# Kernel optimization log

Hardware: AMD Instinct MI355X
Metric: run time of the kernel (lower is better)

Reference implementation:

```python
import jax, jax.numpy as jnp
import numpy as np
from jax import lax

# Model constants (from init_kwargs)
N_B, N_T, N_IN, N_REC, N_OUT = 64, 1000, 80, 512, 20
DT, TAU_M, TAU_O = 1.0, 20.0, 20.0
ALPHA = float(np.exp(-DT / TAU_M))   # membrane leak
KAPPA = float(np.exp(-DT / TAU_O))   # output leak
THR = 1.0
B_O = 0.0
GAIN = (0.5, 0.1, 0.5)


def setup_inputs() -> dict:
    key = jax.random.key(0)
    k = jax.random.split(key, 5)
    x = jax.random.normal(k[0], (N_B, N_T, N_IN), jnp.float32)
    # kaiming_normal_ (fan_in mode, std = sqrt(2/fan_in)) scaled by gain
    w_in = jax.random.normal(k[1], (N_REC, N_IN), jnp.float32) * (np.sqrt(2.0 / N_IN) * GAIN[0])
    w_rec = jax.random.normal(k[2], (N_REC, N_REC), jnp.float32) * (np.sqrt(2.0 / N_REC) * GAIN[1])
    w_out = jax.random.normal(k[3], (N_OUT, N_REC), jnp.float32) * (np.sqrt(2.0 / N_REC) * GAIN[2])
    # per-step torch.randn noise, materialized deterministically
    noise = jax.random.normal(k[4], (N_T, N_B, N_REC), jnp.float32)
    # full-length sequences: pack/pad roundtrip becomes identity
    seq_lengths = jnp.full((N_B,), N_T, dtype=jnp.int32)
    return {"x": x, "w_in": w_in, "w_rec": w_rec, "w_out": w_out,
            "noise": noise, "seq_lengths": seq_lengths}


def reference(x, w_in, w_rec, w_out, noise, seq_lengths):
    """LIF spiking RNN forward (inference path, do_training=False).

    x:     (B, T, n_in)
    noise: (T, B, n_rec)  -- the per-step torch.randn injected into v
    Returns (softmax_vo (B,T,n_out), vo (T,B,n_out)) as in the torch module.
    """
    n_b, n_t, _ = x.shape
    n_rec = w_rec.shape[0]
    n_out = w_out.shape[0]
    dtype = x.dtype

    # zero the recurrent self-connections (w_rec *= 1 - eye)
    w_rec_m = w_rec * (1.0 - jnp.eye(n_rec, dtype=w_rec.dtype))

    # padded inputs are zero beyond seq_lengths; here all lengths == n_t so
    # the pack/pad roundtrip is identity. mask anyway for faithfulness.
    t_idx = jnp.arange(n_t)[None, :, None]                     # (1,T,1)
    x_padded = jnp.where(t_idx < seq_lengths[:, None, None], x, 0.0)

    def step(carry, inp):
        v, z, vo = carry
        x_t, noise_t1 = inp
        # v[t+1] = alpha*v[t] + z[t]@w_rec.T + x[t]@w_in.T - z[t]*thr + noise
        v_new = (ALPHA * v
                 + z @ w_rec_m.T
                 + x_t @ w_in.T
                 - z * THR
                 + noise_t1)
        z_new = (v_new > THR).astype(dtype)          # hard threshold spike
        vo_new = KAPPA * vo + z_new @ w_out.T + B_O  # leaky readout
        return (v_new, z_new, vo_new), vo_new

    init = (jnp.zeros((n_b, n_rec), dtype),
            jnp.zeros((n_b, n_rec), dtype),
            jnp.zeros((n_b, n_out), dtype))
    # loop t = 0 .. n_t-2 consumes x[:, t] and noise[t+1]
    xs = (jnp.swapaxes(x_padded, 0, 1)[:-1], noise[1:])
    _, vo_seq = lax.scan(step, init, xs)             # (T-1, B, n_out)

    vo = jnp.concatenate([jnp.zeros((1, n_b, n_out), dtype), vo_seq], axis=0)  # (T,B,O)
    softmax_vo = jax.nn.softmax(jnp.transpose(vo, (1, 0, 2)), axis=2)          # (B,T,O)
    return softmax_vo, vo
```

## Files before the change

kernel.cpp:

```cpp
#include <hip/hip_runtime.h>

#define N_B   64
#define N_T   1000
#define N_IN  80
#define N_REC 512
#define N_OUT 20
#define THR 1.0f

constexpr float ALPHA = 0.9512294245007140f;
constexpr float KAPPA = 0.9512294245007140f;

__global__ void k_transpose(const float* __restrict__ w_rec, float* __restrict__ wT) {
    int i = blockIdx.x * blockDim.x + threadIdx.x;
    if (i >= 513 * N_REC) return;
    int j = i >> 9;
    int r = i & 511;
    float v = 0.0f;
    if (j < N_REC && r != j) v = w_rec[r * N_REC + j];
    wT[i] = v;
}

__global__ __launch_bounds__(512, 2) void k_inj(
    const float* __restrict__ x, const float* __restrict__ w_in,
    const float* __restrict__ noise, const int* __restrict__ seq,
    float* __restrict__ inj, int t0, int t1)
{
    const int r = threadIdx.x;
    float wreg[N_IN];
#pragma unroll
    for (int i = 0; i < N_IN; ++i) wreg[i] = w_in[r * N_IN + i];

    const int P = (t1 - t0) * N_B;
    const int stride = gridDim.x;

    auto nz = [&](int p) -> float {
        int pt = p >> 6, b = p & 63, t = t0 + pt;
        return __builtin_nontemporal_load(noise + ((size_t)t * N_B + b) * N_REC + r);
    };

    int p = blockIdx.x;
    float nxt = (p < P) ? nz(p) : 0.0f;
    for (; p < P; p += stride) {
        float acc = nxt;
        if (p + stride < P) nxt = nz(p + stride);
        int pt = p >> 6;
        int b  = p & 63;
        int t  = t0 + pt;
        if (t - 1 < seq[b]) {
            const float* xr = x + ((size_t)b * N_T + (t - 1)) * N_IN;
#pragma unroll
            for (int i = 0; i < N_IN; ++i) acc = fmaf(wreg[i], xr[i], acc);
        }
        inj[(size_t)p * N_REC + r] = acc;
    }
}

__global__ __launch_bounds__(512, 1) void k_scan(
    const float* __restrict__ wT, const float* __restrict__ inj,
    const float* __restrict__ w_out, float* __restrict__ out_vo,
    int t0, int t1,
    float* __restrict__ st_v, unsigned long long* __restrict__ st_zm,
    float* __restrict__ st_vo)
{
    const int b    = blockIdx.x;
    const int tid  = threadIdx.x;
    const int w    = tid >> 6;
    const int lane = tid & 63;
    const int g    = tid >> 7;
    const int c    = tid & 127;
    const unsigned long long lt = (1ull << lane) - 1ull;
    const int DUMMY = N_REC << 11;

    __shared__ int lists[N_REC];
    __shared__ unsigned long long zm[8];
    __shared__ int pc[8];
    __shared__ float4 tmp_part[4][128];
    __shared__ float tmp2[16][21];
    __shared__ alignas(16) float zfp[16 * 36];

    float wvo[32];
    {
        int o = tid >> 4, s = tid & 15;
        if (tid < 320) {
#pragma unroll
            for (int i = 0; i < 32; ++i)
                wvo[i] = w_out[(size_t)o * N_REC + s * 32 + i];
        } else {
#pragma unroll
            for (int i = 0; i < 32; ++i) wvo[i] = 0.0f;
        }
    }

    float v;
    int z;
    float vo = 0.0f;
    int npad = 0;

    if (t0 == 1) {
        v = 0.0f; z = 0;
    } else {
        v = st_v[(size_t)b * N_REC + tid];
        unsigned long long m = st_zm[b * 8 + w];
        z = (int)((m >> lane) & 1ull);
        if (tid < 8) zm[tid] = st_zm[b * 8 + tid];
        if (tid < N_OUT) vo = st_vo[b * N_OUT + tid];
        __syncthreads();
        unsigned long long bm0 = zm[w];
        if (lane == 0) pc[w] = __popcll(bm0);
        __syncthreads();
        int basep = 0, ntot = 0;
#pragma unroll
        for (int ww = 0; ww < 8; ++ww) {
            int s_ = pc[ww];
            if (ww < w) basep += s_;
            ntot += s_;
        }
        if (z) lists[basep + __popcll(bm0 & lt)] = tid << 11;
        npad = (ntot + 31) & ~31;
        { int i = ntot + tid; if (i < npad) lists[i] = DUMMY; }
        __syncthreads();
    }

    float injn = __builtin_nontemporal_load(inj + ((size_t)0 * N_B + b) * N_REC + tid);

    for (int t = t0; t < t1; ++t) {
        float injv = injn;

        float4 acc; acc.x = 0.0f; acc.y = 0.0f; acc.z = 0.0f; acc.w = 0.0f;
        {
            const int q = npad >> 2;
            if (q > 0) {
                int jv  = lists[g * q + lane];
                int jv2 = (q > 64) ? lists[g * q + 64 + (lane & 63)] : 0;
                const char* wb = (const char*)wT + (c << 4);
                const int nb = q >> 3;
                float4 vA[8];
#pragma unroll
                for (int u = 0; u < 8; ++u) {
                    int off = __builtin_amdgcn_readlane(jv, u);
                    vA[u] = *(const float4*)(wb + off);
                }
                for (int k = 1; k < nb; ++k) {
                    float4 vB[8];
#pragma unroll
                    for (int u = 0; u < 8; ++u) {
                        int ug = (k << 3) + u;
                        int off = (ug < 64)
                            ? __builtin_amdgcn_readlane(jv,  ug)
                            : __builtin_amdgcn_readlane(jv2, ug - 64);
                        vB[u] = *(const float4*)(wb + off);
                    }
#pragma unroll
                    for (int u = 0; u < 8; ++u) {
                        acc.x += vA[u].x; acc.y += vA[u].y;
                        acc.z += vA[u].z; acc.w += vA[u].w;
                        vA[u] = vB[u];
                    }
                }
#pragma unroll
                for (int u = 0; u < 8; ++u) {
                    acc.x += vA[u].x; acc.y += vA[u].y;
                    acc.z += vA[u].z; acc.w += vA[u].w;
                }
            }
        }
        if (t > t0 && tid < 320) {
            int o = tid >> 4, s = tid & 15;
            const float4* zp = (const float4*)(zfp + s * 36);
            float sa = 0.0f;
#pragma unroll
            for (int i = 0; i < 8; ++i) {
                float4 zv = zp[i];
                sa = fmaf(wvo[4 * i + 0], zv.x, sa);
                sa = fmaf(wvo[4 * i + 1], zv.y, sa);
                sa = fmaf(wvo[4 * i + 2], zv.z, sa);
                sa = fmaf(wvo[4 * i + 3], zv.w, sa);
            }
            tmp2[s][o] = sa;
        }
        tmp_part[g][c] = acc;

        if (t + 1 < t1)
            injn = __builtin_nontemporal_load(
                inj + ((size_t)(t + 1 - t0) * N_B + b) * N_REC + tid);

        __syncthreads();

        {
            const float* tp = (const float*)tmp_part;
            float accn = tp[tid] + tp[512 + tid] + tp[1024 + tid] + tp[1536 + tid];
            v = ALPHA * v + accn + injv - (z ? THR : 0.0f);
            z = v > THR;
            zfp[(tid >> 5) * 36 + (tid & 31)] = z ? 1.0f : 0.0f;
        }
        unsigned long long bm = __ballot(z);
        if (lane == 0) { zm[w] = bm; pc[w] = __popcll(bm); }
        if (t > t0 && tid < N_OUT) {
            float s = 0.0f;
#pragma unroll
            for (int ss = 0; ss < 16; ++ss) s += tmp2[ss][tid];
            vo = KAPPA * vo + s;
            out_vo[((size_t)(t - 1) * N_B + b) * N_OUT + tid] = vo;
        }
        __syncthreads();

        {
            int basep = 0, ntot = 0;
#pragma unroll
            for (int ww = 0; ww < 8; ++ww) {
                int s_ = pc[ww];
                if (ww < w) basep += s_;
                ntot += s_;
            }
            if (z) lists[basep + __popcll(bm & lt)] = tid << 11;
            int npn = (ntot + 31) & ~31;
            { int i = ntot + tid; if (i < npn) lists[i] = DUMMY; }
            npad = npn;
        }
        __syncthreads();
    }

    if (tid < 320) {
        int o = tid >> 4, s = tid & 15;
        const float4* zp = (const float4*)(zfp + s * 36);
        float sa = 0.0f;
#pragma unroll
        for (int i = 0; i < 8; ++i) {
            float4 zv = zp[i];
            sa = fmaf(wvo[4 * i + 0], zv.x, sa);
            sa = fmaf(wvo[4 * i + 1], zv.y, sa);
            sa = fmaf(wvo[4 * i + 2], zv.z, sa);
            sa = fmaf(wvo[4 * i + 3], zv.w, sa);
        }
        tmp2[s][o] = sa;
    }
    __syncthreads();
    if (tid < N_OUT) {
        float s = 0.0f;
#pragma unroll
        for (int ss = 0; ss < 16; ++ss) s += tmp2[ss][tid];
        vo = KAPPA * vo + s;
        out_vo[((size_t)(t1 - 1) * N_B + b) * N_OUT + tid] = vo;
        st_vo[b * N_OUT + tid] = vo;
    }

    st_v[(size_t)b * N_REC + tid] = v;
    if (lane == 0) st_zm[b * 8 + w] = zm[w];
}

__global__ void k_softmax(const float* __restrict__ vo_seq,
                          float* __restrict__ out_sm,
                          float* __restrict__ out_vo0)
{
    int idx = blockIdx.x * blockDim.x + threadIdx.x;
    if (idx >= N_B * N_T) return;
    int b = idx / N_T;
    int t = idx - b * N_T;
    float vals[N_OUT];
    if (t == 0) {
#pragma unroll
        for (int o = 0; o < N_OUT; ++o) {
            vals[o] = 0.0f;
            out_vo0[(size_t)b * N_OUT + o] = 0.0f;
        }
    } else {
#pragma unroll
        for (int o = 0; o < N_OUT; ++o)
            vals[o] = vo_seq[((size_t)t * N_B + b) * N_OUT + o];
    }
    float mx = vals[0];
#pragma unroll
    for (int o = 1; o < N_OUT; ++o) mx = fmaxf(mx, vals[o]);
    float s = 0.0f;
#pragma unroll
    for (int o = 0; o < N_OUT; ++o) { vals[o] = expf(vals[o] - mx); s += vals[o]; }
    float inv = 1.0f / s;
#pragma unroll
    for (int o = 0; o < N_OUT; ++o)
        out_sm[((size_t)b * N_T + t) * N_OUT + o] = vals[o] * inv;
}

extern "C" void kernel_launch(void* const* d_in, const int* in_sizes, int n_in,
                              void* d_out, int out_size, void* d_ws, size_t ws_size,
                              hipStream_t stream)
{
    (void)in_sizes; (void)n_in; (void)out_size;
    const float* x     = (const float*)d_in[0];
    const float* w_in  = (const float*)d_in[1];
    const float* w_rec = (const float*)d_in[2];
    const float* w_out = (const float*)d_in[3];
    const float* noise = (const float*)d_in[4];
    const int*   seq   = (const int*)d_in[5];

    float* out    = (float*)d_out;
    float* out_sm = out;
    float* out_vo = out + (size_t)N_B * N_T * N_OUT;

    char* ws = (char*)d_ws;
    float* wT = (float*)ws;
    size_t off = (size_t)513 * N_REC * sizeof(float);
    float* st_v = (float*)(ws + off);                off += (size_t)N_B * N_REC * sizeof(float);
    unsigned long long* st_zm = (unsigned long long*)(ws + off); off += (size_t)N_B * 8 * sizeof(unsigned long long);
    float* st_vo = (float*)(ws + off);               off += (size_t)N_B * N_OUT * sizeof(float);
    off = (off + 255) & ~(size_t)255;
    float* inj = (float*)(ws + off);

    size_t avail = (ws_size > off) ? (ws_size - off) : 0;
    size_t step_bytes = (size_t)N_B * N_REC * sizeof(float);
    long max_steps = (long)(avail / step_bytes);
    int tchunk = (int)((max_steps > (N_T - 1)) ? (N_T - 1) : max_steps);
    if (tchunk < 1) tchunk = 1;

    k_transpose<<<dim3((513 * N_REC + 255) / 256), dim3(256), 0, stream>>>(w_rec, wT);

    for (int t0 = 1; t0 < N_T; t0 += tchunk) {
        int t1 = t0 + tchunk; if (t1 > N_T) t1 = N_T;
        k_inj<<<dim3(512), dim3(512), 0, stream>>>(x, w_in, noise, seq, inj, t0, t1);
        k_scan<<<dim3(N_B), dim3(512), 0, stream>>>(wT, inj, w_out, out_vo,
                                                    t0, t1, st_v, st_zm, st_vo);
    }

    k_softmax<<<dim3((N_B * N_T + 255) / 256), dim3(256), 0, stream>>>(out_vo, out_sm, out_vo);
}
```

Baseline: 2.625 ms.

## Split each batch row's recurrent scan across two blocks with spike-mask exchange

```diff
diff --git a/kernel.cpp b/kernel.cpp
--- a/kernel.cpp
+++ b/kernel.cpp
@@ -10,8 +10,10 @@
 constexpr float ALPHA = 0.9512294245007140f;
 constexpr float KAPPA = 0.9512294245007140f;
 
-__global__ void k_transpose(const float* __restrict__ w_rec, float* __restrict__ wT) {
+__global__ void k_transpose(const float* __restrict__ w_rec, float* __restrict__ wT,
+                            unsigned long long* __restrict__ ex) {
     int i = blockIdx.x * blockDim.x + threadIdx.x;
+    if (i < 64 * 2 * 2 * 8) ex[i] = 0ull;
     if (i >= 513 * N_REC) return;
     int j = i >> 9;
     int r = i & 511;
@@ -60,113 +62,108 @@
     const float* __restrict__ w_out, float* __restrict__ out_vo,
     int t0, int t1,
     float* __restrict__ st_v, unsigned long long* __restrict__ st_zm,
-    float* __restrict__ st_vo)
+    float* __restrict__ st_vo, unsigned long long* __restrict__ ex)
 {
-    const int b    = blockIdx.x;
+    const int bid  = blockIdx.x;
+    const int b    = bid & 63;
+    const int sh   = bid >> 6;
+    const int cbase = sh << 8;
     const int tid  = threadIdx.x;
     const int w    = tid >> 6;
     const int lane = tid & 63;
-    const int g    = tid >> 7;
-    const int c    = tid & 127;
     const unsigned long long lt = (1ull << lane) - 1ull;
     const int DUMMY = N_REC << 11;
 
     __shared__ int lists[N_REC];
     __shared__ unsigned long long zm[8];
-    __shared__ int pc[8];
-    __shared__ float4 tmp_part[4][128];
+    __shared__ float4 tmp_part[8][64];
     __shared__ float tmp2[16][21];
     __shared__ alignas(16) float zfp[16 * 36];
 
     float wvo[32];
     {
-        int o = tid >> 4, s = tid & 15;
+        int o = tid >> 4, s16 = tid & 15;
         if (tid < 320) {
 #pragma unroll
             for (int i = 0; i < 32; ++i)
-                wvo[i] = w_out[(size_t)o * N_REC + s * 32 + i];
+                wvo[i] = w_out[(size_t)o * N_REC + s16 * 32 + i];
         } else {
 #pragma unroll
             for (int i = 0; i < 32; ++i) wvo[i] = 0.0f;
         }
     }
 
-    float v;
-    int z;
+    float v = 0.0f;
+    int zloc = 0;
     float vo = 0.0f;
     int npad = 0;
 
-    if (t0 == 1) {
-        v = 0.0f; z = 0;
-    } else {
-        v = st_v[(size_t)b * N_REC + tid];
-        unsigned long long m = st_zm[b * 8 + w];
-        z = (int)((m >> lane) & 1ull);
+    if (t0 > 1) {
+        if (tid < 256) v = st_v[(size_t)b * N_REC + cbase + tid];
         if (tid < 8) zm[tid] = st_zm[b * 8 + tid];
-        if (tid < N_OUT) vo = st_vo[b * N_OUT + tid];
-        __syncthreads();
-        unsigned long long bm0 = zm[w];
-        if (lane == 0) pc[w] = __popcll(bm0);
-        __syncthreads();
+        if (tid >= 256 && tid < 256 + N_OUT) vo = st_vo[b * N_OUT + (tid - 256)];
+        __syncthreads();
+        if (tid < 256)
+            zloc = (int)((zm[(cbase + tid) >> 6] >> (tid & 63)) & 1ull);
         int basep = 0, ntot = 0;
 #pragma unroll
         for (int ww = 0; ww < 8; ++ww) {
-            int s_ = pc[ww];
-            if (ww < w) basep += s_;
-            ntot += s_;
-        }
-        if (z) lists[basep + __popcll(bm0 & lt)] = tid << 11;
+            int c_ = __popcll(zm[ww]);
+            if (ww < w) basep += c_;
+            ntot += c_;
+        }
+        unsigned long long bmw = zm[w];
+        if ((bmw >> lane) & 1ull) lists[basep + __popcll(bmw & lt)] = tid << 11;
         npad = (ntot + 31) & ~31;
         { int i = ntot + tid; if (i < npad) lists[i] = DUMMY; }
         __syncthreads();
     }
 
-    float injn = __builtin_nontemporal_load(inj + ((size_t)0 * N_B + b) * N_REC + tid);
+    float injn = 0.0f;
+    if (tid < 256)
+        injn = __builtin_nontemporal_load(
+            inj + ((size_t)0 * N_B + b) * N_REC + cbase + tid);
 
     for (int t = t0; t < t1; ++t) {
         float injv = injn;
 
         float4 acc; acc.x = 0.0f; acc.y = 0.0f; acc.z = 0.0f; acc.w = 0.0f;
         {
-            const int q = npad >> 2;
+            const int q = npad >> 3;
             if (q > 0) {
-                int jv  = lists[g * q + lane];
-                int jv2 = (q > 64) ? lists[g * q + 64 + (lane & 63)] : 0;
-                const char* wb = (const char*)wT + (c << 4);
-                const int nb = q >> 3;
-                float4 vA[8];
-#pragma unroll
-                for (int u = 0; u < 8; ++u) {
+                int jv = lists[w * q + lane];
+                const char* wb = (const char*)wT + (sh << 10) + (lane << 4);
+                const int nb = q >> 2;
+                float4 vA[4];
+#pragma unroll
+                for (int u = 0; u < 4; ++u) {
                     int off = __builtin_amdgcn_readlane(jv, u);
                     vA[u] = *(const float4*)(wb + off);
                 }
-                for (int k = 1; k < nb; ++k) {
-                    float4 vB[8];
-#pragma unroll
-                    for (int u = 0; u < 8; ++u) {
-                        int ug = (k << 3) + u;
-                        int off = (ug < 64)
-                            ? __builtin_amdgcn_readlane(jv,  ug)
-                            : __builtin_amdgcn_readlane(jv2, ug - 64);
+                for (int kb = 1; kb < nb; ++kb) {
+                    float4 vB[4];
+#pragma unroll
+                    for (int u = 0; u < 4; ++u) {
+                        int off = __builtin_amdgcn_readlane(jv, (kb << 2) + u);
                         vB[u] = *(const float4*)(wb + off);
                     }
 #pragma unroll
-                    for (int u = 0; u < 8; ++u) {
+                    for (int u = 0; u < 4; ++u) {
                         acc.x += vA[u].x; acc.y += vA[u].y;
                         acc.z += vA[u].z; acc.w += vA[u].w;
                         vA[u] = vB[u];
                     }
                 }
 #pragma unroll
-                for (int u = 0; u < 8; ++u) {
+                for (int u = 0; u < 4; ++u) {
                     acc.x += vA[u].x; acc.y += vA[u].y;
                     acc.z += vA[u].z; acc.w += vA[u].w;
                 }
             }
         }
         if (t > t0 && tid < 320) {
-            int o = tid >> 4, s = tid & 15;
-            const float4* zp = (const float4*)(zfp + s * 36);
+            int o = tid >> 4, s16 = tid & 15;
+            const float4* zp = (const float4*)(zfp + s16 * 36);
             float sa = 0.0f;
 #pragma unroll
             for (int i = 0; i < 8; ++i) {
@@ -176,31 +173,52 @@
                 sa = fmaf(wvo[4 * i + 2], zv.z, sa);
                 sa = fmaf(wvo[4 * i + 3], zv.w, sa);
             }
-            tmp2[s][o] = sa;
-        }
-        tmp_part[g][c] = acc;
-
-        if (t + 1 < t1)
+            tmp2[s16][o] = sa;
+        }
+        tmp_part[w][lane] = acc;
+
+        if (tid < 256 && t + 1 < t1)
             injn = __builtin_nontemporal_load(
-                inj + ((size_t)(t + 1 - t0) * N_B + b) * N_REC + tid);
-
-        __syncthreads();
-
-        {
+                inj + ((size_t)(t + 1 - t0) * N_B + b) * N_REC + cbase + tid);
+
+        __syncthreads();
+
+        if (tid < 256) {
             const float* tp = (const float*)tmp_part;
-            float accn = tp[tid] + tp[512 + tid] + tp[1024 + tid] + tp[1536 + tid];
-            v = ALPHA * v + accn + injv - (z ? THR : 0.0f);
-            z = v > THR;
-            zfp[(tid >> 5) * 36 + (tid & 31)] = z ? 1.0f : 0.0f;
-        }
-        unsigned long long bm = __ballot(z);
-        if (lane == 0) { zm[w] = bm; pc[w] = __popcll(bm); }
-        if (t > t0 && tid < N_OUT) {
-            float s = 0.0f;
-#pragma unroll
-            for (int ss = 0; ss < 16; ++ss) s += tmp2[ss][tid];
-            vo = KAPPA * vo + s;
-            out_vo[((size_t)(t - 1) * N_B + b) * N_OUT + tid] = vo;
+            float accn = injv;
+#pragma unroll
+            for (int gg = 0; gg < 8; ++gg) accn += tp[gg * 256 + tid];
+            v = ALPHA * v + accn - (zloc ? THR : 0.0f);
+            zloc = v > THR;
+        }
+        unsigned long long bm = __ballot(zloc);
+        if (w < 4 && lane == 0) zm[sh * 4 + w] = bm;
+        __syncthreads();
+
+        if (tid == 0) {
+            const int par = t & 1;
+            unsigned long long* myslot = ex + (size_t)(((((b << 1) | sh) << 1) | par) * 8);
+            unsigned long long* pslot  = ex + (size_t)(((((b << 1) | (1 - sh)) << 1) | par) * 8);
+            unsigned long long w0 = zm[sh * 4 + 0], w1 = zm[sh * 4 + 1];
+            unsigned long long w2 = zm[sh * 4 + 2], w3 = zm[sh * 4 + 3];
+            __hip_atomic_store(myslot + 0, w0, __ATOMIC_RELAXED, __HIP_MEMORY_SCOPE_AGENT);
+            __hip_atomic_store(myslot + 1, w1, __ATOMIC_RELAXED, __HIP_MEMORY_SCOPE_AGENT);
+            __hip_atomic_store(myslot + 2, w2, __ATOMIC_RELAXED, __HIP_MEMORY_SCOPE_AGENT);
+            __hip_atomic_store(myslot + 3, w3, __ATOMIC_RELAXED, __HIP_MEMORY_SCOPE_AGENT);
+            __hip_atomic_store(myslot + 4, (unsigned long long)t,
+                               __ATOMIC_RELEASE, __HIP_MEMORY_SCOPE_AGENT);
+            while (__hip_atomic_load(pslot + 4, __ATOMIC_ACQUIRE,
+                                     __HIP_MEMORY_SCOPE_AGENT) < (unsigned long long)t) {}
+            zm[(1 - sh) * 4 + 0] = __hip_atomic_load(pslot + 0, __ATOMIC_RELAXED, __HIP_MEMORY_SCOPE_AGENT);
+            zm[(1 - sh) * 4 + 1] = __hip_atomic_load(pslot + 1, __ATOMIC_RELAXED, __HIP_MEMORY_SCOPE_AGENT);
+            zm[(1 - sh) * 4 + 2] = __hip_atomic_load(pslot + 2, __ATOMIC_RELAXED, __HIP_MEMORY_SCOPE_AGENT);
+            zm[(1 - sh) * 4 + 3] = __hip_atomic_load(pslot + 3, __ATOMIC_RELAXED, __HIP_MEMORY_SCOPE_AGENT);
+        } else if (tid >= 256 && tid < 256 + N_OUT && t > t0) {
+            float sum = 0.0f;
+#pragma unroll
+            for (int ss = 0; ss < 16; ++ss) sum += tmp2[ss][tid - 256];
+            vo = KAPPA * vo + sum;
+            out_vo[((size_t)(t - 1) * N_B + b) * N_OUT + (tid - 256)] = vo;
         }
         __syncthreads();
 
@@ -208,21 +226,24 @@
             int basep = 0, ntot = 0;
 #pragma unroll
             for (int ww = 0; ww < 8; ++ww) {
-                int s_ = pc[ww];
-                if (ww < w) basep += s_;
-                ntot += s_;
+                int c_ = __popcll(zm[ww]);
+                if (ww < w) basep += c_;
+                ntot += c_;
             }
-            if (z) lists[basep + __popcll(bm & lt)] = tid << 11;
+            unsigned long long bmw = zm[w];
+            if ((bmw >> lane) & 1ull) lists[basep + __popcll(bmw & lt)] = tid << 11;
             int npn = (ntot + 31) & ~31;
             { int i = ntot + tid; if (i < npn) lists[i] = DUMMY; }
             npad = npn;
+            zfp[(tid >> 5) * 36 + (tid & 31)] =
+                ((zm[tid >> 6] >> (tid & 63)) & 1ull) ? 1.0f : 0.0f;
         }
         __syncthreads();
     }
 
     if (tid < 320) {
-        int o = tid >> 4, s = tid & 15;
-        const float4* zp = (const float4*)(zfp + s * 36);
+        int o = tid >> 4, s16 = tid & 15;
+        const float4* zp = (const float4*)(zfp + s16 * 36);
         float sa = 0.0f;
 #pragma unroll
         for (int i = 0; i < 8; ++i) {
@@ -232,20 +253,20 @@
             sa = fmaf(wvo[4 * i + 2], zv.z, sa);
             sa = fmaf(wvo[4 * i + 3], zv.w, sa);
         }
-        tmp2[s][o] = sa;
+        tmp2[s16][o] = sa;
     }
     __syncthreads();
-    if (tid < N_OUT) {
-        float s = 0.0f;
-#pragma unroll
-        for (int ss = 0; ss < 16; ++ss) s += tmp2[ss][tid];
-        vo = KAPPA * vo + s;
-        out_vo[((size_t)(t1 - 1) * N_B + b) * N_OUT + tid] = vo;
-        st_vo[b * N_OUT + tid] = vo;
-    }
-
-    st_v[(size_t)b * N_REC + tid] = v;
-    if (lane == 0) st_zm[b * 8 + w] = zm[w];
+    if (tid >= 256 && tid < 256 + N_OUT) {
+        float sum = 0.0f;
+#pragma unroll
+        for (int ss = 0; ss < 16; ++ss) sum += tmp2[ss][tid - 256];
+        vo = KAPPA * vo + sum;
+        out_vo[((size_t)(t1 - 1) * N_B + b) * N_OUT + (tid - 256)] = vo;
+        st_vo[b * N_OUT + (tid - 256)] = vo;
+    }
+
+    if (tid < 256) st_v[(size_t)b * N_REC + cbase + tid] = v;
+    if (tid < 8) st_zm[b * 8 + tid] = zm[tid];
 }
 
 __global__ void k_softmax(const float* __restrict__ vo_seq,
@@ -299,9 +320,13 @@
     char* ws = (char*)d_ws;
     float* wT = (float*)ws;
     size_t off = (size_t)513 * N_REC * sizeof(float);
+    off = (off + 255) & ~(size_t)255;
     float* st_v = (float*)(ws + off);                off += (size_t)N_B * N_REC * sizeof(float);
     unsigned long long* st_zm = (unsigned long long*)(ws + off); off += (size_t)N_B * 8 * sizeof(unsigned long long);
     float* st_vo = (float*)(ws + off);               off += (size_t)N_B * N_OUT * sizeof(float);
+    off = (off + 255) & ~(size_t)255;
+    unsigned long long* ex = (unsigned long long*)(ws + off);
+    off += (size_t)64 * 2 * 2 * 8 * sizeof(unsigned long long);
     off = (off + 255) & ~(size_t)255;
     float* inj = (float*)(ws + off);
 
@@ -311,13 +336,13 @@
     int tchunk = (int)((max_steps > (N_T - 1)) ? (N_T - 1) : max_steps);
     if (tchunk < 1) tchunk = 1;
 
-    k_transpose<<<dim3((513 * N_REC + 255) / 256), dim3(256), 0, stream>>>(w_rec, wT);
+    k_transpose<<<dim3((513 * N_REC + 255) / 256), dim3(256), 0, stream>>>(w_rec, wT, ex);
 
     for (int t0 = 1; t0 < N_T; t0 += tchunk) {
         int t1 = t0 + tchunk; if (t1 > N_T) t1 = N_T;
         k_inj<<<dim3(512), dim3(512), 0, stream>>>(x, w_in, noise, seq, inj, t0, t1);
-        k_scan<<<dim3(N_B), dim3(512), 0, stream>>>(wT, inj, w_out, out_vo,
-                                                    t0, t1, st_v, st_zm, st_vo);
+        k_scan<<<dim3(2 * N_B), dim3(512), 0, stream>>>(wT, inj, w_out, out_vo,
+                                                        t0, t1, st_v, st_zm, st_vo, ex);
     }
 
     k_softmax<<<dim3((N_B * N_T + 255) / 256), dim3(256), 0, stream>>>(out_vo, out_sm, out_vo);
```

After: 4.709 ms. 1.79x slower.

## Run recurrent matmul on MFMA with register-resident split-bf16 weights across blocks

Applied to the files above, without the earlier changes.

```diff
diff --git a/kernel.cpp b/kernel.cpp
--- a/kernel.cpp
+++ b/kernel.cpp
@@ -10,14 +10,56 @@
 constexpr float ALPHA = 0.9512294245007140f;
 constexpr float KAPPA = 0.9512294245007140f;
 
-__global__ void k_transpose(const float* __restrict__ w_rec, float* __restrict__ wT) {
-    int i = blockIdx.x * blockDim.x + threadIdx.x;
-    if (i >= 513 * N_REC) return;
-    int j = i >> 9;
-    int r = i & 511;
-    float v = 0.0f;
-    if (j < N_REC && r != j) v = w_rec[r * N_REC + j];
-    wT[i] = v;
+typedef short bf16x8 __attribute__((ext_vector_type(8)));
+typedef float f32x4  __attribute__((ext_vector_type(4)));
+
+__device__ __forceinline__ void barrier_lgkm() {
+    asm volatile("s_waitcnt lgkmcnt(0)" ::: "memory");
+    __builtin_amdgcn_s_barrier();
+}
+
+__device__ __forceinline__ unsigned short f2bf(float f) {
+    unsigned u = __builtin_bit_cast(unsigned, f);
+    return (unsigned short)((u + 0x7FFFu + ((u >> 16) & 1u)) >> 16);
+}
+__device__ __forceinline__ float bf2f(unsigned short h) {
+    return __builtin_bit_cast(float, (unsigned)h << 16);
+}
+
+__global__ void k_prep(const float* __restrict__ w_rec, unsigned* __restrict__ wPack,
+                       unsigned long long* __restrict__ ex) {
+    int gid = blockIdx.x * 256 + threadIdx.x;
+    if (gid < 32 * 2 * 32) ex[gid] = 0ull;
+    if (gid >= 8 * 2 * 4 * 8 * 3 * 64) return;
+    int lane = gid & 63;
+    int fg   = gid >> 6;
+    int s    = fg % 3;
+    int q    = fg / 3;
+    int ksl  = q & 7;
+    int nt   = (q >> 3) & 3;
+    int kh   = (q >> 5) & 1;
+    int ns   = q >> 6;
+    int n  = ns * 64 + nt * 16 + (lane & 15);
+    int kb = (kh * 8 + ksl) * 32 + 4 * (lane >> 4);
+    unsigned u[4];
+#pragma unroll
+    for (int j = 0; j < 4; ++j) {
+        unsigned short h2v[2];
+#pragma unroll
+        for (int e = 0; e < 2; ++e) {
+            int i = j * 2 + e;
+            int k = kb + ((i >> 2) << 4) + (i & 3);
+            float w0 = (k == n) ? 0.0f : w_rec[(size_t)n * N_REC + k];
+            unsigned short h1 = f2bf(w0);
+            float r1 = w0 - bf2f(h1);
+            unsigned short hm = f2bf(r1);
+            float r2 = r1 - bf2f(hm);
+            unsigned short hl = f2bf(r2);
+            h2v[e] = (s == 0) ? h1 : (s == 1) ? hm : hl;
+        }
+        u[j] = (unsigned)h2v[0] | ((unsigned)h2v[1] << 16);
+    }
+    ((uint4*)wPack)[gid] = make_uint4(u[0], u[1], u[2], u[3]);
 }
 
 __global__ __launch_bounds__(512, 2) void k_inj(
@@ -56,196 +98,226 @@
 }
 
 __global__ __launch_bounds__(512, 1) void k_scan(
-    const float* __restrict__ wT, const float* __restrict__ inj,
-    const float* __restrict__ w_out, float* __restrict__ out_vo,
+    const unsigned* __restrict__ wPack, const float* __restrict__ inj,
+    const float* __restrict__ w_out, float* __restrict__ vop,
     int t0, int t1,
-    float* __restrict__ st_v, unsigned long long* __restrict__ st_zm,
-    float* __restrict__ st_vo)
+    float* __restrict__ st_v, unsigned long long* __restrict__ st_bal,
+    float* __restrict__ st_vop, unsigned long long* __restrict__ ex)
 {
-    const int b    = blockIdx.x;
+    const int bid  = blockIdx.x;
+    const int bg   = bid >> 3;
+    const int ns   = bid & 7;
     const int tid  = threadIdx.x;
-    const int w    = tid >> 6;
+    const int wv   = tid >> 6;
     const int lane = tid & 63;
-    const int g    = tid >> 7;
-    const int c    = tid & 127;
-    const unsigned long long lt = (1ull << lane) - 1ull;
-    const int DUMMY = N_REC << 11;
-
-    __shared__ int lists[N_REC];
-    __shared__ unsigned long long zm[8];
-    __shared__ int pc[8];
-    __shared__ float4 tmp_part[4][128];
-    __shared__ float tmp2[16][21];
-    __shared__ alignas(16) float zfp[16 * 36];
-
-    float wvo[32];
+    const int nt   = wv & 3;
+    const int kh   = wv >> 2;
+
+    __shared__ uint4 zlds[64 * 16];
+    __shared__ unsigned bal32[8][4][4][2];
+    __shared__ f32x4 red[4][64];
+    __shared__ alignas(16) float wo[20][68];
+
+    bf16x8 wreg[24];
     {
-        int o = tid >> 4, s = tid & 15;
-        if (tid < 320) {
-#pragma unroll
-            for (int i = 0; i < 32; ++i)
-                wvo[i] = w_out[(size_t)o * N_REC + s * 32 + i];
+        const uint4* wp = (const uint4*)wPack + (size_t)(((ns * 2 + kh) * 4 + nt) * 24) * 64;
+#pragma unroll
+        for (int j = 0; j < 24; ++j)
+            wreg[j] = __builtin_bit_cast(bf16x8, wp[j * 64 + lane]);
+    }
+    for (int idx = tid; idx < 20 * 64; idx += 512)
+        wo[idx >> 6][idx & 63] = w_out[(size_t)(idx >> 6) * N_REC + ns * 64 + (idx & 63)];
+
+    float v0 = 0, v1 = 0, v2 = 0, v3 = 0;
+    int zprev = 0;
+    unsigned long long bm0 = 0, bm1 = 0, bm2 = 0, bm3 = 0;
+    float vo0 = 0, vo1 = 0;
+
+    if (t0 == 1) {
+        if (tid < 256) (&bal32[0][0][0][0])[tid] = 0u;
+    } else {
+        if (tid < 256) {
+            unsigned long long wd = st_bal[bg * 128 + (tid >> 1)];
+            (&bal32[0][0][0][0])[tid] = (unsigned)(wd >> (32 * (tid & 1)));
+        }
+        if (wv < 4) {
+            f32x4 sv = ((const f32x4*)st_v)[bid * 256 + tid];
+            v0 = sv[0]; v1 = sv[1]; v2 = sv[2]; v3 = sv[3];
         } else {
-#pragma unroll
-            for (int i = 0; i < 32; ++i) wvo[i] = 0.0f;
-        }
-    }
-
-    float v;
-    int z;
-    float vo = 0.0f;
-    int npad = 0;
-
-    if (t0 == 1) {
-        v = 0.0f; z = 0;
+            int q = tid - 256;
+            vo0 = st_vop[bid * 320 + q];
+            if (q < 64) vo1 = st_vop[bid * 320 + 256 + q];
+        }
+    }
+    __syncthreads();
+    if (wv < 4) {
+        int h = lane >> 5, sh = lane & 31;
+#pragma unroll
+        for (int r = 0; r < 4; ++r)
+            zprev |= (int)((bal32[ns][wv][r][h] >> sh) & 1u) << r;
+    }
+
+    auto bmsel = [&](int r) -> unsigned long long {
+        return (r == 0) ? bm0 : (r == 1) ? bm1 : (r == 2) ? bm2 : bm3;
+    };
+    auto injaddr = [&](int trel, int r) -> const float* {
+        return inj + ((size_t)trel * 64 + bg * 16 + (lane >> 4) * 4 + r) * N_REC
+                   + ns * 64 + nt * 16 + (lane & 15);
+    };
+    auto vo_step = [&](int slot) {
+        int q = tid - 256;
+        int m = q & 15, o = q >> 4;
+        unsigned long long mask = 0;
+#pragma unroll
+        for (int w2 = 0; w2 < 4; ++w2) {
+            unsigned long long wd = (unsigned long long)bal32[ns][w2][m & 3][0]
+                                  | ((unsigned long long)bal32[ns][w2][m & 3][1] << 32);
+            mask |= ((wd >> ((m >> 2) * 16)) & 0xFFFFull) << (16 * w2);
+        }
+        float s0 = 0.f, s1 = 0.f;
+#pragma unroll
+        for (int jj = 0; jj < 16; ++jj) {
+            unsigned nib = (unsigned)(mask >> (4 * jj)) & 0xFu;
+            float4 wa = *(const float4*)&wo[o][jj * 4];
+            s0 += (nib & 1u) ? wa.x : 0.f;
+            s0 += (nib & 2u) ? wa.y : 0.f;
+            s0 += (nib & 4u) ? wa.z : 0.f;
+            s0 += (nib & 8u) ? wa.w : 0.f;
+            if (o < 4) {
+                float4 wb = *(const float4*)&wo[o + 16][jj * 4];
+                s1 += (nib & 1u) ? wb.x : 0.f;
+                s1 += (nib & 2u) ? wb.y : 0.f;
+                s1 += (nib & 4u) ? wb.z : 0.f;
+                s1 += (nib & 8u) ? wb.w : 0.f;
+            }
+        }
+        vo0 = KAPPA * vo0 + s0;
+        size_t sidx = ((size_t)slot * 64 + bg * 16 + m) * 160;
+        vop[sidx + o * 8 + ns] = vo0;
+        if (o < 4) { vo1 = KAPPA * vo1 + s1; vop[sidx + (o + 16) * 8 + ns] = vo1; }
+    };
+
+    float in0 = 0, in1 = 0, in2 = 0, in3 = 0;
+    if (wv < 4) {
+        in0 = __builtin_nontemporal_load(injaddr(0, 0));
+        in1 = __builtin_nontemporal_load(injaddr(0, 1));
+        in2 = __builtin_nontemporal_load(injaddr(0, 2));
+        in3 = __builtin_nontemporal_load(injaddr(0, 3));
+    }
+
+    for (int t = t0; t < t1; ++t) {
+        float iv0 = in0, iv1 = in1, iv2 = in2, iv3 = in3;
+
+        unsigned long long spec = 0; unsigned long long* slot = nullptr;
+        if (t > t0) {
+            if (wv < 4 && lane < 8) {
+                int r = lane >> 1, hf = lane & 1;
+                bal32[ns][wv][r][hf] = (unsigned)(bmsel(r) >> (32 * hf));
+            }
+            if (tid < 224) {
+                int pi = tid >> 5; int ns2 = pi + (pi >= ns);
+                slot = ex + ((size_t)((bg * 8 + ns2) * 2 + ((t - 1) & 1)) * 32 + (tid & 31));
+                spec = atomicAdd(slot, 0ull);
+            }
+        }
+        if (wv < 4 && t + 1 < t1) {
+            in0 = __builtin_nontemporal_load(injaddr(t + 1 - t0, 0));
+            in1 = __builtin_nontemporal_load(injaddr(t + 1 - t0, 1));
+            in2 = __builtin_nontemporal_load(injaddr(t + 1 - t0, 2));
+            in3 = __builtin_nontemporal_load(injaddr(t + 1 - t0, 3));
+        }
+        if (t > t0 && tid < 224) {
+            int guard = 0;
+            while ((unsigned)(spec >> 32) != (unsigned)(t - 1) && ++guard < 100000)
+                spec = atomicAdd(slot, 0ull);
+            int sl = tid & 31; int pi = tid >> 5; int ns2 = pi + (pi >= ns);
+            bal32[ns2][sl >> 3][(sl >> 1) & 3][sl & 1] = (unsigned)spec;
+        }
+        barrier_lgkm();
+
+#pragma unroll
+        for (int tk = 0; tk < 2; ++tk) {
+            int task = tid + tk * 512;
+            int m = task & 15, kl = task >> 4;
+            int ks = kl >> 2, lg = kl & 3;
+            int bit = ((m >> 2) << 4) + (lg << 2);
+            int h = bit >> 5, sh = bit & 31;
+            unsigned nib1 = (bal32[ks >> 1][(ks & 1) * 2][m & 3][h] >> sh) & 0xFu;
+            unsigned nib2 = (bal32[ks >> 1][(ks & 1) * 2 + 1][m & 3][h] >> sh) & 0xFu;
+            uint4 o;
+            o.x = ((nib1 & 1u) ? 0x3F80u : 0u) | ((nib1 & 2u) ? 0x3F800000u : 0u);
+            o.y = ((nib1 & 4u) ? 0x3F80u : 0u) | ((nib1 & 8u) ? 0x3F800000u : 0u);
+            o.z = ((nib2 & 1u) ? 0x3F80u : 0u) | ((nib2 & 2u) ? 0x3F800000u : 0u);
+            o.w = ((nib2 & 4u) ? 0x3F80u : 0u) | ((nib2 & 8u) ? 0x3F800000u : 0u);
+            zlds[kl * 16 + m] = o;
+        }
+        barrier_lgkm();
+
+        f32x4 acc = {0.f, 0.f, 0.f, 0.f};
+#pragma unroll
+        for (int ksl = 0; ksl < 8; ++ksl) {
+            int ks = kh * 8 + ksl;
+            bf16x8 a = __builtin_bit_cast(bf16x8,
+                zlds[(ks * 4 + (lane >> 4)) * 16 + (lane & 15)]);
+            acc = __builtin_amdgcn_mfma_f32_16x16x32_bf16(a, wreg[ksl * 3 + 0], acc, 0, 0, 0);
+            acc = __builtin_amdgcn_mfma_f32_16x16x32_bf16(a, wreg[ksl * 3 + 1], acc, 0, 0, 0);
+            acc = __builtin_amdgcn_mfma_f32_16x16x32_bf16(a, wreg[ksl * 3 + 2], acc, 0, 0, 0);
+        }
+        if (kh == 1) red[nt][lane] = acc;
+        barrier_lgkm();
+
+        if (wv < 4) {
+            f32x4 rs = red[wv][lane];
+            float vn0 = ALPHA * v0 + (acc[0] + rs[0]) + iv0 - ((zprev & 1) ? THR : 0.f);
+            float vn1 = ALPHA * v1 + (acc[1] + rs[1]) + iv1 - ((zprev & 2) ? THR : 0.f);
+            float vn2 = ALPHA * v2 + (acc[2] + rs[2]) + iv2 - ((zprev & 4) ? THR : 0.f);
+            float vn3 = ALPHA * v3 + (acc[3] + rs[3]) + iv3 - ((zprev & 8) ? THR : 0.f);
+            v0 = vn0; v1 = vn1; v2 = vn2; v3 = vn3;
+            int z0 = vn0 > THR, z1 = vn1 > THR, z2 = vn2 > THR, z3 = vn3 > THR;
+            zprev = z0 | (z1 << 1) | (z2 << 2) | (z3 << 3);
+            bm0 = __ballot(z0); bm1 = __ballot(z1); bm2 = __ballot(z2); bm3 = __ballot(z3);
+            if (lane < 8) {
+                unsigned long long word =
+                    ((unsigned long long)(unsigned)t << 32) |
+                    (unsigned long long)(unsigned)(bmsel(lane >> 1) >> (32 * (lane & 1)));
+                atomicExch(ex + ((size_t)((bg * 8 + ns) * 2 + (t & 1)) * 32 + wv * 8 + lane),
+                           word);
+            }
+        } else if (t > t0) {
+            vo_step(t - 1 - t0);
+        }
+        barrier_lgkm();
+    }
+
+    if (wv < 4 && lane < 8) {
+        int r = lane >> 1, hf = lane & 1;
+        bal32[ns][wv][r][hf] = (unsigned)(bmsel(r) >> (32 * hf));
+    }
+    barrier_lgkm();
+    if (wv >= 4) {
+        vo_step(t1 - 1 - t0);
+        int q = tid - 256;
+        st_vop[bid * 320 + q] = vo0;
+        if (q < 64) st_vop[bid * 320 + 256 + q] = vo1;
     } else {
-        v = st_v[(size_t)b * N_REC + tid];
-        unsigned long long m = st_zm[b * 8 + w];
-        z = (int)((m >> lane) & 1ull);
-        if (tid < 8) zm[tid] = st_zm[b * 8 + tid];
-        if (tid < N_OUT) vo = st_vo[b * N_OUT + tid];
-        __syncthreads();
-        unsigned long long bm0 = zm[w];
-        if (lane == 0) pc[w] = __popcll(bm0);
-        __syncthreads();
-        int basep = 0, ntot = 0;
-#pragma unroll
-        for (int ww = 0; ww < 8; ++ww) {
-            int s_ = pc[ww];
-            if (ww < w) basep += s_;
-            ntot += s_;
-        }
-        if (z) lists[basep + __popcll(bm0 & lt)] = tid << 11;
-        npad = (ntot + 31) & ~31;
-        { int i = ntot + tid; if (i < npad) lists[i] = DUMMY; }
-        __syncthreads();
-    }
-
-    float injn = __builtin_nontemporal_load(inj + ((size_t)0 * N_B + b) * N_REC + tid);
-
-    for (int t = t0; t < t1; ++t) {
-        float injv = injn;
-
-        float4 acc; acc.x = 0.0f; acc.y = 0.0f; acc.z = 0.0f; acc.w = 0.0f;
-        {
-            const int q = npad >> 2;
-            if (q > 0) {
-                int jv  = lists[g * q + lane];
-                int jv2 = (q > 64) ? lists[g * q + 64 + (lane & 63)] : 0;
-                const char* wb = (const char*)wT + (c << 4);
-                const int nb = q >> 3;
-                float4 vA[8];
-#pragma unroll
-                for (int u = 0; u < 8; ++u) {
-                    int off = __builtin_amdgcn_readlane(jv, u);
-                    vA[u] = *(const float4*)(wb + off);
-                }
-                for (int k = 1; k < nb; ++k) {
-                    float4 vB[8];
-#pragma unroll
-                    for (int u = 0; u < 8; ++u) {
-                        int ug = (k << 3) + u;
-                        int off = (ug < 64)
-                            ? __builtin_amdgcn_readlane(jv,  ug)
-                            : __builtin_amdgcn_readlane(jv2, ug - 64);
-                        vB[u] = *(const float4*)(wb + off);
-                    }
-#pragma unroll
-                    for (int u = 0; u < 8; ++u) {
-                        acc.x += vA[u].x; acc.y += vA[u].y;
-                        acc.z += vA[u].z; acc.w += vA[u].w;
-                        vA[u] = vB[u];
-                    }
-                }
-#pragma unroll
-                for (int u = 0; u < 8; ++u) {
-                    acc.x += vA[u].x; acc.y += vA[u].y;
-                    acc.z += vA[u].z; acc.w += vA[u].w;
-                }
-            }
-        }
-        if (t > t0 && tid < 320) {
-            int o = tid >> 4, s = tid & 15;
-            const float4* zp = (const float4*)(zfp + s * 36);
-            float sa = 0.0f;
-#pragma unroll
-            for (int i = 0; i < 8; ++i) {
-                float4 zv = zp[i];
-                sa = fmaf(wvo[4 * i + 0], zv.x, sa);
-                sa = fmaf(wvo[4 * i + 1], zv.y, sa);
-                sa = fmaf(wvo[4 * i + 2], zv.z, sa);
-                sa = fmaf(wvo[4 * i + 3], zv.w, sa);
-            }
-            tmp2[s][o] = sa;
-        }
-        tmp_part[g][c] = acc;
-
-        if (t + 1 < t1)
-            injn = __builtin_nontemporal_load(
-                inj + ((size_t)(t + 1 - t0) * N_B + b) * N_REC + tid);
-
-        __syncthreads();
-
-        {
-            const float* tp = (const float*)tmp_part;
-            float accn = tp[tid] + tp[512 + tid] + tp[1024 + tid] + tp[1536 + tid];
-            v = ALPHA * v + accn + injv - (z ? THR : 0.0f);
-            z = v > THR;
-            zfp[(tid >> 5) * 36 + (tid & 31)] = z ? 1.0f : 0.0f;
-        }
-        unsigned long long bm = __ballot(z);
-        if (lane == 0) { zm[w] = bm; pc[w] = __popcll(bm); }
-        if (t > t0 && tid < N_OUT) {
-            float s = 0.0f;
-#pragma unroll
-            for (int ss = 0; ss < 16; ++ss) s += tmp2[ss][tid];
-            vo = KAPPA * vo + s;
-            out_vo[((size_t)(t - 1) * N_B + b) * N_OUT + tid] = vo;
-        }
-        __syncthreads();
-
-        {
-            int basep = 0, ntot = 0;
-#pragma unroll
-            for (int ww = 0; ww < 8; ++ww) {
-                int s_ = pc[ww];
-                if (ww < w) basep += s_;
-                ntot += s_;
-            }
-            if (z) lists[basep + __popcll(bm & lt)] = tid << 11;
-            int npn = (ntot + 31) & ~31;
-            { int i = ntot + tid; if (i < npn) lists[i] = DUMMY; }
-            npad = npn;
-        }
-        __syncthreads();
-    }
-
-    if (tid < 320) {
-        int o = tid >> 4, s = tid & 15;
-        const float4* zp = (const float4*)(zfp + s * 36);
-        float sa = 0.0f;
-#pragma unroll
-        for (int i = 0; i < 8; ++i) {
-            float4 zv = zp[i];
-            sa = fmaf(wvo[4 * i + 0], zv.x, sa);
-            sa = fmaf(wvo[4 * i + 1], zv.y, sa);
-            sa = fmaf(wvo[4 * i + 2], zv.z, sa);
-            sa = fmaf(wvo[4 * i + 3], zv.w, sa);
-        }
-        tmp2[s][o] = sa;
-    }
-    __syncthreads();
-    if (tid < N_OUT) {
-        float s = 0.0f;
-#pragma unroll
-        for (int ss = 0; ss < 16; ++ss) s += tmp2[ss][tid];
-        vo = KAPPA * vo + s;
-        out_vo[((size_t)(t1 - 1) * N_B + b) * N_OUT + tid] = vo;
-        st_vo[b * N_OUT + tid] = vo;
-    }
-
-    st_v[(size_t)b * N_REC + tid] = v;
-    if (lane == 0) st_zm[b * 8 + w] = zm[w];
+        f32x4 sv; sv[0] = v0; sv[1] = v1; sv[2] = v2; sv[3] = v3;
+        ((f32x4*)st_v)[bid * 256 + tid] = sv;
+        if (lane < 4)
+            st_bal[bg * 128 + ns * 16 + wv * 4 + lane] = bmsel(lane);
+    }
+}
+
+__global__ void k_vored(const float* __restrict__ vop, float* __restrict__ out_vo,
+                        int t0, int t1) {
+    int idx = blockIdx.x * 256 + threadIdx.x;
+    int n = (t1 - t0) * N_B * N_OUT;
+    if (idx >= n) return;
+    int s = idx / (N_B * N_OUT);
+    int rem = idx - s * (N_B * N_OUT);
+    int b = rem / N_OUT, o = rem - b * N_OUT;
+    const float* p = vop + ((size_t)s * 64 + b) * 160 + o * 8;
+    float acc = p[0] + p[1] + p[2] + p[3] + p[4] + p[5] + p[6] + p[7];
+    out_vo[((size_t)(t0 + s) * N_B + b) * N_OUT + o] = acc;
 }
 
 __global__ void k_softmax(const float* __restrict__ vo_seq,
@@ -297,27 +369,35 @@
     float* out_vo = out + (size_t)N_B * N_T * N_OUT;
 
     char* ws = (char*)d_ws;
-    float* wT = (float*)ws;
-    size_t off = (size_t)513 * N_REC * sizeof(float);
-    float* st_v = (float*)(ws + off);                off += (size_t)N_B * N_REC * sizeof(float);
-    unsigned long long* st_zm = (unsigned long long*)(ws + off); off += (size_t)N_B * 8 * sizeof(unsigned long long);
-    float* st_vo = (float*)(ws + off);               off += (size_t)N_B * N_OUT * sizeof(float);
+    unsigned* wPack = (unsigned*)ws;
+    size_t off = (size_t)98304 * 16;
     off = (off + 255) & ~(size_t)255;
-    float* inj = (float*)(ws + off);
+    float* st_v = (float*)(ws + off);                off += (size_t)32 * 256 * 16;
+    unsigned long long* st_bal = (unsigned long long*)(ws + off); off += (size_t)4 * 128 * 8;
+    float* st_vop = (float*)(ws + off);              off += (size_t)32 * 320 * 4;
+    off = (off + 255) & ~(size_t)255;
+    unsigned long long* ex = (unsigned long long*)(ws + off);
+    off += (size_t)32 * 2 * 32 * 8;
+    off = (off + 255) & ~(size_t)255;
 
     size_t avail = (ws_size > off) ? (ws_size - off) : 0;
-    size_t step_bytes = (size_t)N_B * N_REC * sizeof(float);
-    long max_steps = (long)(avail / step_bytes);
+    size_t inj_step = (size_t)N_B * N_REC * sizeof(float);
+    size_t vop_step = (size_t)N_B * N_OUT * 8 * sizeof(float);
+    long max_steps = (long)(avail / (inj_step + vop_step));
     int tchunk = (int)((max_steps > (N_T - 1)) ? (N_T - 1) : max_steps);
     if (tchunk < 1) tchunk = 1;
-
-    k_transpose<<<dim3((513 * N_REC + 255) / 256), dim3(256), 0, stream>>>(w_rec, wT);
+    float* inj = (float*)(ws + off);
+    float* vop = (float*)(ws + off + (size_t)tchunk * inj_step);
+
+    k_prep<<<dim3(384), dim3(256), 0, stream>>>(w_rec, wPack, ex);
 
     for (int t0 = 1; t0 < N_T; t0 += tchunk) {
         int t1 = t0 + tchunk; if (t1 > N_T) t1 = N_T;
         k_inj<<<dim3(512), dim3(512), 0, stream>>>(x, w_in, noise, seq, inj, t0, t1);
-        k_scan<<<dim3(N_B), dim3(512), 0, stream>>>(wT, inj, w_out, out_vo,
-                                                    t0, t1, st_v, st_zm, st_vo);
+        k_scan<<<dim3(32), dim3(512), 0, stream>>>(wPack, inj, w_out, vop,
+                                                   t0, t1, st_v, st_bal, st_vop, ex);
+        int nred = (t1 - t0) * N_B * N_OUT;
+        k_vored<<<dim3((nred + 255) / 256), dim3(256), 0, stream>>>(vop, out_vo, t0, t1);
     }
 
     k_softmax<<<dim3((N_B * N_T + 255) / 256), dim3(256), 0, stream>>>(out_vo, out_sm, out_vo);
```

New measurement: 3.777 ms. 43.9% more time.
